# Optimization experiments

Measured on AMD Instinct MI355X. Metric: run time of the kernel, lower is better.

The kernel has to match this reference:

```python
import jax, jax.numpy as jnp
import numpy as np

N_NODES = 50000
N_EDGES = 600000
IN_F, HID_F, OUT_F = 128, 128, 64


def setup_inputs() -> dict:
    key = jax.random.key(0)
    ks = jax.random.split(key, 7)
    features = jax.random.normal(ks[0], (N_NODES, IN_F), jnp.float32)
    W1 = jax.random.normal(ks[1], (IN_F, HID_F), jnp.float32) / np.sqrt(IN_F)
    b1 = jnp.zeros((HID_F,), jnp.float32)
    W2 = jax.random.normal(ks[2], (HID_F, OUT_F), jnp.float32) / np.sqrt(HID_F)
    b2 = jnp.zeros((OUT_F,), jnp.float32)
    edge_src = jax.random.randint(ks[3], (N_EDGES,), 0, N_NODES, jnp.int32)
    edge_dst = jax.random.randint(ks[4], (N_EDGES,), 0, N_NODES, jnp.int32)
    return {"features": features, "W1": W1, "b1": b1, "W2": W2, "b2": b2,
            "edge_src": edge_src, "edge_dst": edge_dst}


def _graph_conv(h, W, b, edge_src, edge_dst, norm_src, norm_dst, n_nodes):
    # DGL GraphConv, norm='both': D_in^{-1/2} A D_out^{-1/2} (h W) + b
    # Apply W first (linear commutes with the linear aggregation) to minimize
    # the size of the gathered edge tensor when out <= in.
    h = (h * norm_src[:, None]) @ W                       # [N, d_out]
    agg = jax.ops.segment_sum(h[edge_src], edge_dst, num_segments=n_nodes)
    return agg * norm_dst[:, None] + b


def reference(features, W1, b1, W2, b2, edge_src, edge_dst):
    n_nodes = features.shape[0]
    ones = jnp.ones(edge_src.shape[0], features.dtype)
    out_deg = jax.ops.segment_sum(ones, edge_src, num_segments=n_nodes)
    in_deg = jax.ops.segment_sum(ones, edge_dst, num_segments=n_nodes)
    norm_src = jnp.clip(out_deg, 1.0) ** -0.5             # source-side D_out^{-1/2}
    norm_dst = jnp.clip(in_deg, 1.0) ** -0.5              # dest-side   D_in^{-1/2}
    h = _graph_conv(features, W1, b1, edge_src, edge_dst, norm_src, norm_dst, n_nodes)
    h = jax.nn.relu(h)
    h = _graph_conv(h, W2, b2, edge_src, edge_dst, norm_src, norm_dst, n_nodes)
    return h
```

## Files before the change

### kernel.cpp

```cpp
#include <hip/hip_runtime.h>


typedef unsigned short u16;
typedef unsigned int u32;
typedef short s16x8 __attribute__((ext_vector_type(8)));
typedef float f32x4 __attribute__((ext_vector_type(4)));
typedef u32 u32x4 __attribute__((ext_vector_type(4)));

__device__ __forceinline__ float bf2f(u16 u) {
    return __uint_as_float((u32)u << 16);
}
__device__ __forceinline__ u16 f2bf(float f) {
    u32 u = __float_as_uint(f);
    u += 0x7fff + ((u >> 16) & 1);
    return (u16)(u >> 16);
}


__global__ __launch_bounds__(256) void hist_part(const int* __restrict__ src,
                                                 const int* __restrict__ dst,
                                                 u32* __restrict__ part) {
    __shared__ u32 cnt[6250];
    const int s = blockIdx.x;
    const int r = blockIdx.y;
    const int z = blockIdx.z;
    const int lo = r * 12500;
    for (int t = threadIdx.x; t < 6250; t += 256) cnt[t] = 0;
    __syncthreads();
    const int* ids = z ? dst : src;
    const int base = s * 37500;
    for (int e0 = base; e0 < base + 37500; e0 += 1024) {
        int idx[4];
#pragma unroll
        for (int k = 0; k < 4; ++k) {
            int e = e0 + k * 256 + threadIdx.x;
            idx[k] = (e < base + 37500) ? ids[e] : -1;
        }
#pragma unroll
        for (int k = 0; k < 4; ++k) {
            unsigned local = (unsigned)(idx[k] - lo);
            if (local < 12500u)
                atomicAdd(&cnt[local >> 1], 1u << ((local & 1) * 16));
        }
    }
    __syncthreads();
    u32* out = part + (size_t)(z * 16 + s) * 25000 + r * 6250;
    for (int t = threadIdx.x; t < 6250; t += 256) out[t] = cnt[t];
}

__global__ __launch_bounds__(256) void reduce_norm_sniff(const u32* __restrict__ part,
                                                         int* __restrict__ degd,
                                                         float* __restrict__ ns,
                                                         float* __restrict__ nd,
                                                         int* __restrict__ bsum,
                                                         const u16* __restrict__ X16,
                                                         int* __restrict__ flag) {
    __shared__ int sh[256];
    if (blockIdx.x == 0) {
        u16 v = X16[threadIdx.x * 2];
        int e = (v >> 7) & 0xFF;
        sh[threadIdx.x] = (e >= 0x30 && e <= 0x47) ? 1 : 0;
        __syncthreads();
        for (int off = 128; off > 0; off >>= 1) {
            if (threadIdx.x < off) sh[threadIdx.x] += sh[threadIdx.x + off];
            __syncthreads();
        }
        if (threadIdx.x == 0) *flag = (sh[0] >= 128) ? 1 : 0;
        __syncthreads();
    }
    int i = blockIdx.x * 256 + threadIdx.x;
    u32 a = 0, b = 0;
    if (i < 50000) {
        const int w = i >> 1, h = (i & 1) * 16;
#pragma unroll
        for (int s = 0; s < 16; ++s) {
            a += (part[(size_t)s * 25000 + w] >> h) & 0xffffu;
            b += (part[(size_t)(16 + s) * 25000 + w] >> h) & 0xffffu;
        }
        degd[i] = (int)b;
        ns[i] = rsqrtf((float)(a > 1 ? a : 1));
        nd[i] = rsqrtf((float)(b > 1 ? b : 1));
    }
    sh[threadIdx.x] = (i < 50000) ? (int)b : 0;
    __syncthreads();
    for (int off = 128; off > 0; off >>= 1) {
        if (threadIdx.x < off) sh[threadIdx.x] += sh[threadIdx.x + off];
        __syncthreads();
    }
    if (threadIdx.x == 0) bsum[blockIdx.x] = sh[0];
}

__global__ __launch_bounds__(256) void rowptr_scan(const int* __restrict__ degd,
                                                   const int* __restrict__ bsum,
                                                   int* __restrict__ rp,
                                                   int* __restrict__ cur,
                                                   int n, int nb) {
    __shared__ int sb[256];
    __shared__ int sh[256];
    const int t = threadIdx.x;
    sb[t] = (t < nb && t < (int)blockIdx.x) ? bsum[t] : 0;
    int i = blockIdx.x * 256 + t;
    int v = (i < n) ? degd[i] : 0;
    sh[t] = v;
    __syncthreads();
    for (int off = 128; off > 0; off >>= 1) {
        if (t < off) sb[t] += sb[t + off];
        __syncthreads();
    }
    const int boff = sb[0];
    for (int off = 1; off < 256; off <<= 1) {
        int x = (t >= off) ? sh[t - off] : 0;
        __syncthreads();
        sh[t] += x;
        __syncthreads();
    }
    if (i < n) {
        int e = boff + sh[t] - v;
        rp[i] = e;
        cur[i] = e;
        if (i == n - 1) rp[n] = e + v;
    }
}

__global__ __launch_bounds__(256) void fill_kernel(const int* __restrict__ src,
                                                   const int* __restrict__ dst,
                                                   int* __restrict__ cur,
                                                   int* __restrict__ col, int n) {
    int i = blockIdx.x * 256 + threadIdx.x;
    if (i < n) {
        int pos = atomicAdd(&cur[dst[i]], 1);
        col[pos] = src[i];
    }
}

template <int FO, bool X_ALWAYS_BF16>
__global__ __launch_bounds__(256) void gemm_mfma(const void* __restrict__ Xv,
                                                 const void* __restrict__ Wv,
                                                 const int* __restrict__ flagp,
                                                 const float* __restrict__ ns,
                                                 u16* __restrict__ Ylo,
                                                 u16* __restrict__ Yhi,
                                                 int split, int nrows) {
    constexpr int NCT = FO / 64;
    __shared__ __align__(16) u32 Xs[64 * 68];
    const int flag = *flagp;
    const int tid = threadIdx.x;
    const int nb = blockIdx.x * 64;

    const bool xbf = X_ALWAYS_BF16 ? true : (flag != 0);
    if (xbf) {
        const u32* Xg = (const u32*)Xv;
        for (int t = tid; t < 64 * 64; t += 256) {
            int row = t >> 6, cp = t & 63;
            int r = nb + row;
            Xs[row * 68 + cp] = (r < nrows) ? Xg[(size_t)r * 64 + cp] : 0u;
        }
    } else {
        const float* Xg = (const float*)Xv;
        for (int t = tid; t < 64 * 64; t += 256) {
            int row = t >> 6, cp = t & 63;
            int r = nb + row;
            u32 lo = 0, hi = 0;
            if (r < nrows) {
                lo = f2bf(Xg[(size_t)r * 128 + 2 * cp]);
                hi = f2bf(Xg[(size_t)r * 128 + 2 * cp + 1]);
            }
            Xs[row * 68 + cp] = lo | (hi << 16);
        }
    }

    const int lane = tid & 63;
    const int wv = tid >> 6;
    const int lr = lane & 15;
    const int g = lane >> 4;
    const int cbase = wv * (FO / 4);

    u32 bf[NCT][4][4];
    if (flag) {
        const u32* Wg = (const u32*)Wv;
#pragma unroll
        for (int c = 0; c < NCT; ++c) {
            const int col = cbase + c * 16 + lr;
            const int ce = col >> 1, sh = (col & 1) * 16;
#pragma unroll
            for (int t = 0; t < 4; ++t)
#pragma unroll
                for (int p = 0; p < 4; ++p) {
                    const int kp = t * 16 + g * 4 + p;
                    u32 lo = (Wg[(size_t)(2 * kp) * (FO / 2) + ce] >> sh) & 0xffffu;
                    u32 hi = (Wg[(size_t)(2 * kp + 1) * (FO / 2) + ce] >> sh) & 0xffffu;
                    bf[c][t][p] = lo | (hi << 16);
                }
        }
    } else {
        const float* Wg = (const float*)Wv;
#pragma unroll
        for (int c = 0; c < NCT; ++c) {
            const int col = cbase + c * 16 + lr;
#pragma unroll
            for (int t = 0; t < 4; ++t)
#pragma unroll
                for (int p = 0; p < 4; ++p) {
                    const int kp = t * 16 + g * 4 + p;
                    u32 lo = f2bf(Wg[(size_t)(2 * kp) * FO + col]);
                    u32 hi = f2bf(Wg[(size_t)(2 * kp + 1) * FO + col]);
                    bf[c][t][p] = lo | (hi << 16);
                }
        }
    }
    __syncthreads();

    union U4 { u32x4 u; s16x8 s; };
#pragma unroll
    for (int rt = 0; rt < 4; ++rt) {
        U4 a[4];
#pragma unroll
        for (int t = 0; t < 4; ++t)
            a[t].u = *(const u32x4*)&Xs[(rt * 16 + lr) * 68 + t * 16 + g * 4];
        const int rq = nb + rt * 16 + g * 4;
        float nsv[4];
#pragma unroll
        for (int q = 0; q < 4; ++q) nsv[q] = ns[rq + q];
#pragma unroll
        for (int c = 0; c < NCT; ++c) {
            f32x4 acc = {0.f, 0.f, 0.f, 0.f};
#pragma unroll
            for (int t = 0; t < 4; ++t) {
                U4 b;
                b.u = (u32x4){bf[c][t][0], bf[c][t][1], bf[c][t][2], bf[c][t][3]};
                acc = __builtin_amdgcn_mfma_f32_16x16x32_bf16(a[t].s, b.s, acc,
                                                              0, 0, 0);
            }
            const int cc = cbase + c * 16 + lr;
#pragma unroll
            for (int q = 0; q < 4; ++q) {
                int r = rq + q;
                if (r < nrows) {
                    u16* Y = (r < split) ? (Ylo + (size_t)r * FO)
                                         : (Yhi + (size_t)(r - split) * FO);
                    Y[cc] = f2bf(acc[q] * nsv[q]);
                }
            }
        }
    }
}

__global__ __launch_bounds__(256) void gather128(const u16* __restrict__ Hlo,
                                                 const u16* __restrict__ Hhi, int split,
                                                 const int* __restrict__ rp,
                                                 const int* __restrict__ col,
                                                 const float* __restrict__ nd,
                                                 const void* __restrict__ bias,
                                                 const int* __restrict__ flagp,
                                                 u16* __restrict__ out, int nnodes) {
    int wv = threadIdx.x >> 6, lane = threadIdx.x & 63;
    int n = blockIdx.x * 4 + wv;
    if (n >= nnodes) return;
    int p0 = rp[n], p1 = rp[n + 1];
    float a0 = 0.f, a1 = 0.f;
    int e = p0;
    for (; e + 8 <= p1; e += 8) {
        u32 u[8];
#pragma unroll
        for (int t = 0; t < 8; ++t) {
            int s = col[e + t];
            const u32* r = (const u32*)((s < split) ? (Hlo + (size_t)s * 128)
                                                    : (Hhi + (size_t)(s - split) * 128));
            u[t] = r[lane];
        }
#pragma unroll
        for (int t = 0; t < 8; ++t) {
            a0 += bf2f((u16)(u[t] & 0xffff));
            a1 += bf2f((u16)(u[t] >> 16));
        }
    }
    for (; e + 4 <= p1; e += 4) {
        u32 u[4];
#pragma unroll
        for (int t = 0; t < 4; ++t) {
            int s = col[e + t];
            const u32* r = (const u32*)((s < split) ? (Hlo + (size_t)s * 128)
                                                    : (Hhi + (size_t)(s - split) * 128));
            u[t] = r[lane];
        }
#pragma unroll
        for (int t = 0; t < 4; ++t) {
            a0 += bf2f((u16)(u[t] & 0xffff));
            a1 += bf2f((u16)(u[t] >> 16));
        }
    }
    for (; e < p1; ++e) {
        int s = col[e];
        const u16* H = (s < split) ? (Hlo + (size_t)s * 128)
                                   : (Hhi + (size_t)(s - split) * 128);
        u32 u = ((const u32*)H)[lane];
        a0 += bf2f((u16)(u & 0xffff));
        a1 += bf2f((u16)(u >> 16));
    }
    int flag = *flagp;
    float bb0 = flag ? bf2f(((const u16*)bias)[lane * 2]) : ((const float*)bias)[lane * 2];
    float bb1 = flag ? bf2f(((const u16*)bias)[lane * 2 + 1]) : ((const float*)bias)[lane * 2 + 1];
    float v = nd[n];
    float o0 = fmaxf(a0 * v + bb0, 0.f);
    float o1 = fmaxf(a1 * v + bb1, 0.f);
    ((u32*)(out + (size_t)n * 128))[lane] = (u32)f2bf(o0) | ((u32)f2bf(o1) << 16);
}

__global__ __launch_bounds__(256) void gather64(const u16* __restrict__ H,
                                                const int* __restrict__ rp,
                                                const int* __restrict__ col,
                                                const float* __restrict__ nd,
                                                const void* __restrict__ bias,
                                                const int* __restrict__ flagp,
                                                void* __restrict__ outv, int nnodes) {
    int wv = threadIdx.x >> 6, lane = threadIdx.x & 63;
    int n = blockIdx.x * 4 + wv;
    if (n >= nnodes) return;
    int p0 = rp[n], p1 = rp[n + 1];
    float a = 0.f;
    int e = p0;
    for (; e + 8 <= p1; e += 8) {
        float f[8];
#pragma unroll
        for (int t = 0; t < 8; ++t)
            f[t] = bf2f(H[(size_t)col[e + t] * 64 + lane]);
#pragma unroll
        for (int t = 0; t < 8; ++t) a += f[t];
    }
    for (; e + 4 <= p1; e += 4) {
        float f[4];
#pragma unroll
        for (int t = 0; t < 4; ++t)
            f[t] = bf2f(H[(size_t)col[e + t] * 64 + lane]);
#pragma unroll
        for (int t = 0; t < 4; ++t) a += f[t];
    }
    for (; e < p1; ++e)
        a += bf2f(H[(size_t)col[e] * 64 + lane]);
    int flag = *flagp;
    float bb = flag ? bf2f(((const u16*)bias)[lane]) : ((const float*)bias)[lane];
    float o = a * nd[n] + bb;
    if (flag)
        ((u16*)outv)[(size_t)n * 64 + lane] = f2bf(o);
    else
        ((float*)outv)[(size_t)n * 64 + lane] = o;
}

extern "C" void kernel_launch(void* const* d_in, const int* in_sizes, int n_in,
                              void* d_out, int out_size, void* d_ws, size_t ws_size,
                              hipStream_t stream) {
    constexpr int N = 50000;
    constexpr int E = 600000;
    constexpr int NB = (N + 255) / 256;
    constexpr int SPLIT = 25000;

    const void* X  = d_in[0];
    const void* W1 = d_in[1];
    const void* b1 = d_in[2];
    const void* W2 = d_in[3];
    const void* b2 = d_in[4];
    const int* esrc = (const int*)d_in[5];
    const int* edst = (const int*)d_in[6];

    char* p = (char*)d_ws;
    auto take = [&](size_t bytes) -> char* {
        char* r = p;
        p += (bytes + 255) & ~(size_t)255;
        return r;
    };
    int* flagp  = (int*)take(256);
    int* deg_d  = (int*)take((size_t)N * 4);
    float* ns   = (float*)take((size_t)N * 4);
    float* nd   = (float*)take((size_t)N * 4);
    int* bsum   = (int*)take((size_t)NB * 4);
    int* rp     = (int*)take((size_t)(N + 1) * 4);
    int* cur    = (int*)take((size_t)N * 4);
    int* col    = (int*)take((size_t)E * 4);
    u16* h0hi   = (u16*)take((size_t)(N - SPLIT) * 128 * 2);
    u16* a2     = (u16*)take((size_t)N * 128 * 2);
    size_t NEED = (size_t)(p - (char*)d_ws);

    if (ws_size < NEED) {
        hipMemsetAsync(d_out, 0, (size_t)out_size * 2, stream);
        return;
    }

    u16* h0lo = (u16*)d_out;

    u32* part = (u32*)a2;

    hist_part<<<dim3(16, 4, 2), 256, 0, stream>>>(esrc, edst, part);
    reduce_norm_sniff<<<NB, 256, 0, stream>>>(part, deg_d, ns, nd, bsum,
                                              (const u16*)X, flagp);
    rowptr_scan<<<NB, 256, 0, stream>>>(deg_d, bsum, rp, cur, N, NB);
    fill_kernel<<<(E + 255) / 256, 256, 0, stream>>>(esrc, edst, cur, col, E);

    gemm_mfma<128, false><<<(N + 63) / 64, 256, 0, stream>>>(
        X, W1, flagp, ns, h0lo, h0hi, SPLIT, N);
    gather128<<<(N + 3) / 4, 256, 0, stream>>>(h0lo, h0hi, SPLIT, rp, col, nd,
                                               b1, flagp, a2, N);

    u16* h1b = h0hi;
    gemm_mfma<64, true><<<(N + 63) / 64, 256, 0, stream>>>(
        a2, W2, flagp, ns, h1b, h1b, N, N);
    gather64<<<(N + 3) / 4, 256, 0, stream>>>(h1b, rp, col, nd, b2, flagp,
                                              d_out, N);

    (void)in_sizes; (void)n_in; (void)out_size;
}
```

Before: 225.8 us.

## Build CSR column array with LDS-local cursors seeded from partial histograms

Replaces the global-atomic CSR fill with a 16x4 grid kernel. Each block owns one edge slice and one 12500-node destination range, and keeps per-node cursors in shared memory. The cursors are seeded from the row pointers plus the earlier slices' per-slice in-degree counts taken from the histogram partials. This removes the global cursor array and the contended global atomics in exchange for shared-memory atomics. Each block now re-reads its whole edge slice's dst array, only 64 blocks run, and the seeding loop reads partials serially.

```diff
diff --git a/kernel.cpp b/kernel.cpp
--- a/kernel.cpp
+++ b/kernel.cpp
@@ -93,7 +93,6 @@
 __global__ __launch_bounds__(256) void rowptr_scan(const int* __restrict__ degd,
                                                    const int* __restrict__ bsum,
                                                    int* __restrict__ rp,
-                                                   int* __restrict__ cur,
                                                    int n, int nb) {
     __shared__ int sb[256];
     __shared__ int sh[256];
@@ -117,19 +116,44 @@
     if (i < n) {
         int e = boff + sh[t] - v;
         rp[i] = e;
-        cur[i] = e;
         if (i == n - 1) rp[n] = e + v;
     }
 }
 
-__global__ __launch_bounds__(256) void fill_kernel(const int* __restrict__ src,
-                                                   const int* __restrict__ dst,
-                                                   int* __restrict__ cur,
-                                                   int* __restrict__ col, int n) {
-    int i = blockIdx.x * 256 + threadIdx.x;
-    if (i < n) {
-        int pos = atomicAdd(&cur[dst[i]], 1);
-        col[pos] = src[i];
+__global__ __launch_bounds__(256) void fill_lds(const int* __restrict__ src,
+                                                const int* __restrict__ dst,
+                                                const int* __restrict__ rp,
+                                                const u32* __restrict__ part,
+                                                int* __restrict__ col) {
+    __shared__ u32 cursor[12500];
+    const int s = blockIdx.x;
+    const int r = blockIdx.y;
+    const int lo = r * 12500;
+    for (int t = threadIdx.x; t < 12500; t += 256) {
+        int i = lo + t;
+        u32 seed = (u32)rp[i];
+        const int w = i >> 1, h = (i & 1) * 16;
+        for (int s2 = 0; s2 < s; ++s2)
+            seed += (part[(size_t)(16 + s2) * 25000 + w] >> h) & 0xffffu;
+        cursor[t] = seed;
+    }
+    __syncthreads();
+    const int base = s * 37500;
+    for (int e0 = base; e0 < base + 37500; e0 += 1024) {
+        int d[4], ev[4];
+#pragma unroll
+        for (int k = 0; k < 4; ++k) {
+            ev[k] = e0 + k * 256 + threadIdx.x;
+            d[k] = (ev[k] < base + 37500) ? dst[ev[k]] : -1;
+        }
+#pragma unroll
+        for (int k = 0; k < 4; ++k) {
+            unsigned local = (unsigned)(d[k] - lo);
+            if (local < 12500u) {
+                u32 pos = atomicAdd(&cursor[local], 1u);
+                col[pos] = src[ev[k]];
+            }
+        }
     }
 }
 
@@ -374,7 +398,6 @@
     float* nd   = (float*)take((size_t)N * 4);
     int* bsum   = (int*)take((size_t)NB * 4);
     int* rp     = (int*)take((size_t)(N + 1) * 4);
-    int* cur    = (int*)take((size_t)N * 4);
     int* col    = (int*)take((size_t)E * 4);
     u16* h0hi   = (u16*)take((size_t)(N - SPLIT) * 128 * 2);
     u16* a2     = (u16*)take((size_t)N * 128 * 2);
@@ -392,8 +415,8 @@
     hist_part<<<dim3(16, 4, 2), 256, 0, stream>>>(esrc, edst, part);
     reduce_norm_sniff<<<NB, 256, 0, stream>>>(part, deg_d, ns, nd, bsum,
                                               (const u16*)X, flagp);
-    rowptr_scan<<<NB, 256, 0, stream>>>(deg_d, bsum, rp, cur, N, NB);
-    fill_kernel<<<(E + 255) / 256, 256, 0, stream>>>(esrc, edst, cur, col, E);
+    rowptr_scan<<<NB, 256, 0, stream>>>(deg_d, bsum, rp, N, NB);
+    fill_lds<<<dim3(16, 4), 256, 0, stream>>>(esrc, edst, rp, part, col);
 
     gemm_mfma<128, false><<<(N + 63) / 64, 256, 0, stream>>>(
         X, W1, flagp, ns, h0lo, h0hi, SPLIT, N);
```

After: 331.3 us. 1.47x slower.
